# Kernel tuning notes

Hardware: AMD Instinct MI355X
Metric: run time of the kernel (lower is better)

The kernel has to match this reference:

```python
import jax, jax.numpy as jnp
import numpy as np

B, F_SIZE, DIM = 2048, 32, 64
LAYER_SIZES = (128, 128)


def setup_inputs() -> dict:
    key = jax.random.key(0)
    k1, k2, k3 = jax.random.split(key, 3)
    inputs = jax.random.normal(k1, (B, F_SIZE, DIM), dtype=jnp.float32)
    # Conv1d(kernel=1) weights: (out_channels, in_channels)
    W0 = jax.random.normal(k2, (128, F_SIZE * F_SIZE), dtype=jnp.float32) * 0.03
    b0 = jnp.zeros((128,), dtype=jnp.float32)
    # split_half -> field_nums[1] = 64 -> in_channels = 64 * 32 = 2048
    W1 = jax.random.normal(k3, (128, 64 * F_SIZE), dtype=jnp.float32) * 0.03
    b1 = jnp.zeros((128,), dtype=jnp.float32)
    return {"inputs": inputs, "W0": W0, "b0": b0, "W1": W1, "b1": b1}


def _cin_forward(inputs, Ws, bs):
    batch, _, dim = inputs.shape
    x0 = inputs
    h = inputs
    finals = []
    n_layers = len(Ws)
    for i in range(n_layers):
        H = h.shape[1]
        M = x0.shape[1]
        # outer-product interaction: (b, H, M, d) -> (b, H*M, d)
        z = jnp.einsum('bhd,bmd->bhmd', h, x0).reshape(batch, H * M, dim)
        # 1x1 conv == per-position channel matmul
        out = jnp.einsum('bcd,oc->bod', z, Ws[i]) + bs[i][None, :, None]
        out = jax.nn.relu(out)
        size = Ws[i].shape[0]
        if i != n_layers - 1:
            # split_half: first half feeds next layer, second half is output
            h = out[:, : size // 2, :]
            finals.append(out[:, size // 2 :, :])
        else:
            finals.append(out)
    result = jnp.concatenate(finals, axis=1)  # (b, 64 + 128, d)
    return jnp.sum(result, axis=-1)           # (b, 192)


def reference(inputs, W0, b0, W1, b1):
    return _cin_forward(inputs, (W0, W1), (b0, b1))
```

## Files before the change

kernel.cpp:

```cpp
#include <hip/hip_runtime.h>


#define BATCH 2048
#define FSZ   32
#define DIM   64
#define K0    1024
#define K1    2048
#define OUTC  192

#define W0_ELEMS (128 * K0)
#define W1_ELEMS (128 * K1)
#define TOT_ELEMS (W0_ELEMS + W1_ELEMS)
#define CVT_THREADS (TOT_ELEMS / 4)

typedef _Float16 v8h __attribute__((ext_vector_type(8)));
typedef _Float16 v4h __attribute__((ext_vector_type(4)));
typedef float    v4f __attribute__((ext_vector_type(4)));

#define XT_PITCH 40

__global__ void convert_w_kernel(const float* __restrict__ W0,
                                 const float* __restrict__ W1,
                                 _Float16* __restrict__ wsw) {
    int t = blockIdx.x * blockDim.x + threadIdx.x;
    if (t >= CVT_THREADS) return;
    int e = t * 4;
    const float* src;
    _Float16* dst;
    if (e < W0_ELEMS) {
        int j0 = e & 7, lane = (e >> 3) & 63, s = (e >> 9) & 7, ks = e >> 12;
        src = W0 + (size_t)(s * 16 + (lane & 15)) * K0
                 + ks * 32 + (lane >> 4) * 8 + j0;
        dst = wsw + e;
    } else {
        int u = e - W0_ELEMS;
        int j0 = u & 7, lane = (u >> 3) & 63, s = (u >> 9) & 7, ks = u >> 12;
        src = W1 + (size_t)(s * 16 + (lane & 15)) * K1
                 + ks * 32 + (lane >> 4) * 8 + j0;
        dst = wsw + W0_ELEMS + u;
    }
    float4 v = *(const float4*)src;
    dst[0] = (_Float16)v.x;
    dst[1] = (_Float16)v.y;
    dst[2] = (_Float16)v.z;
    dst[3] = (_Float16)v.w;
}

__global__ __launch_bounds__(256, 4) void cin_kernel(
    const float* __restrict__ X,
    const float* __restrict__ b0,
    const float* __restrict__ b1,
    const _Float16* __restrict__ Wsw,
    float* __restrict__ out)
{
    __shared__ _Float16 xT[2][DIM * XT_PITCH];
    __shared__ _Float16 xS[2][FSZ * 64];
    __shared__ _Float16 h1S[2][64 * 64];

    const int b0i  = blockIdx.x * 2;
    const int tid  = threadIdx.x;
    const int wave = tid >> 6;
    const int lane = tid & 63;
    const int p    = wave & 1;
    const int rh   = wave >> 1;
    const int quad = lane >> 4;
    const int col  = lane & 15;

    #pragma unroll
    for (int i = 0; i < 4; ++i) {
        int idx = tid + i * 256;
        int pp = idx >> 9, r4 = idx & 511;
        float4 v = *(const float4*)(X + (size_t)(b0i + pp) * (FSZ * DIM) + r4 * 4);
        int m = (r4 * 4) >> 6, d = (r4 * 4) & 63;
        int tq = d >> 4, cc = d & 15;
        _Float16 f0 = (_Float16)v.x, f1 = (_Float16)v.y,
                 f2 = (_Float16)v.z, f3 = (_Float16)v.w;
        xT[pp][(d + 0) * XT_PITCH + m] = f0;
        xT[pp][(d + 1) * XT_PITCH + m] = f1;
        xT[pp][(d + 2) * XT_PITCH + m] = f2;
        xT[pp][(d + 3) * XT_PITCH + m] = f3;
        xS[pp][m * 64 + (cc + 0) * 4 + tq] = f0;
        xS[pp][m * 64 + (cc + 1) * 4 + tq] = f1;
        xS[pp][m * 64 + (cc + 2) * 4 + tq] = f2;
        xS[pp][m * 64 + (cc + 3) * 4 + tq] = f3;
    }
    __syncthreads();

    v8h xv8[4];
    #pragma unroll
    for (int t = 0; t < 4; ++t)
        xv8[t] = *(const v8h*)(&xT[p][(16 * t + col) * XT_PITCH + quad * 8]);

    const _Float16* WbL0 = Wsw + (size_t)rh * 2048 + (size_t)lane * 8;
    const _Float16* Wb   = Wsw + (size_t)(rh * 4) * 512 + (size_t)lane * 8;
    const _Float16* xSp  = &xS[p][col * 4];
    const _Float16* h1Sp = &h1S[p][col * 4];
    (void)WbL0;

    v4f acc[4][4];
    #pragma unroll
    for (int f = 0; f < 4; ++f)
        #pragma unroll
        for (int t = 0; t < 4; ++t) acc[f][t] = (v4f)0.0f;

    {
        v8h aC[4], aN[4];
        v4h svC, svN;
        #pragma unroll
        for (int i = 0; i < 4; ++i) aC[i] = *(const v8h*)(Wb + i * 512);
        svC = *(const v4h*)(xSp);
        #pragma unroll 2
        for (int ks = 0; ks < 32; ++ks) {
            const int kn = (ks + 1) & 31;
            const _Float16* Wn = Wb + (size_t)kn * 4096;
            #pragma unroll
            for (int i = 0; i < 4; ++i) aN[i] = *(const v8h*)(Wn + i * 512);
            svN = *(const v4h*)(xSp + kn * 64);
            __builtin_amdgcn_s_setprio(1);
            #pragma unroll
            for (int t = 0; t < 4; ++t) {
                _Float16 s = svC[t];
                v8h s8 = {s, s, s, s, s, s, s, s};
                v8h bfr = s8 * xv8[t];
                acc[0][t] = __builtin_amdgcn_mfma_f32_16x16x32_f16(aC[0], bfr, acc[0][t], 0, 0, 0);
                acc[1][t] = __builtin_amdgcn_mfma_f32_16x16x32_f16(aC[1], bfr, acc[1][t], 0, 0, 0);
                acc[2][t] = __builtin_amdgcn_mfma_f32_16x16x32_f16(aC[2], bfr, acc[2][t], 0, 0, 0);
                acc[3][t] = __builtin_amdgcn_mfma_f32_16x16x32_f16(aC[3], bfr, acc[3][t], 0, 0, 0);
            }
            __builtin_amdgcn_s_setprio(0);
            #pragma unroll
            for (int i = 0; i < 4; ++i) aC[i] = aN[i];
            svC = svN;
        }
    }

    if (rh == 0) {
        #pragma unroll
        for (int f = 0; f < 4; ++f) {
            #pragma unroll
            for (int reg = 0; reg < 4; ++reg) {
                const int o = f * 16 + quad * 4 + reg;
                const float bias = b0[o];
                v4h pk;
                #pragma unroll
                for (int t = 0; t < 4; ++t) {
                    float v = acc[f][t][reg] + bias;
                    v = v > 0.0f ? v : 0.0f;
                    pk[t] = (_Float16)v;
                }
                *(v4h*)(&h1S[p][o * 64 + col * 4]) = pk;
            }
        }
    } else {
        #pragma unroll
        for (int f = 0; f < 4; ++f) {
            #pragma unroll
            for (int reg = 0; reg < 4; ++reg) {
                const int o = 64 + f * 16 + quad * 4 + reg;
                const float bias = b0[o];
                float s = 0.0f;
                #pragma unroll
                for (int t = 0; t < 4; ++t) {
                    float v = acc[f][t][reg] + bias;
                    s += (v > 0.0f ? v : 0.0f);
                }
                s += __shfl_xor(s, 1);
                s += __shfl_xor(s, 2);
                s += __shfl_xor(s, 4);
                s += __shfl_xor(s, 8);
                if (col == 0) out[(size_t)(b0i + p) * OUTC + (o - 64)] = s;
            }
        }
    }
    __syncthreads();

    #pragma unroll
    for (int f = 0; f < 4; ++f)
        #pragma unroll
        for (int t = 0; t < 4; ++t) acc[f][t] = (v4f)0.0f;

    {
        const _Float16* Wb1 = Wsw + W0_ELEMS + (size_t)(rh * 4) * 512 + (size_t)lane * 8;
        v8h aC[4], aN[4];
        v4h svC, svN;
        #pragma unroll
        for (int i = 0; i < 4; ++i) aC[i] = *(const v8h*)(Wb1 + i * 512);
        svC = *(const v4h*)(h1Sp);
        #pragma unroll 2
        for (int ks = 0; ks < 64; ++ks) {
            const int kn = (ks + 1) & 63;
            const _Float16* Wn = Wb1 + (size_t)kn * 4096;
            #pragma unroll
            for (int i = 0; i < 4; ++i) aN[i] = *(const v8h*)(Wn + i * 512);
            svN = *(const v4h*)(h1Sp + kn * 64);
            __builtin_amdgcn_s_setprio(1);
            #pragma unroll
            for (int t = 0; t < 4; ++t) {
                _Float16 s = svC[t];
                v8h s8 = {s, s, s, s, s, s, s, s};
                v8h bfr = s8 * xv8[t];
                acc[0][t] = __builtin_amdgcn_mfma_f32_16x16x32_f16(aC[0], bfr, acc[0][t], 0, 0, 0);
                acc[1][t] = __builtin_amdgcn_mfma_f32_16x16x32_f16(aC[1], bfr, acc[1][t], 0, 0, 0);
                acc[2][t] = __builtin_amdgcn_mfma_f32_16x16x32_f16(aC[2], bfr, acc[2][t], 0, 0, 0);
                acc[3][t] = __builtin_amdgcn_mfma_f32_16x16x32_f16(aC[3], bfr, acc[3][t], 0, 0, 0);
            }
            __builtin_amdgcn_s_setprio(0);
            #pragma unroll
            for (int i = 0; i < 4; ++i) aC[i] = aN[i];
            svC = svN;
        }
    }

    #pragma unroll
    for (int f = 0; f < 4; ++f) {
        #pragma unroll
        for (int reg = 0; reg < 4; ++reg) {
            const int o = rh * 64 + f * 16 + quad * 4 + reg;
            const float bias = b1[o];
            float s = 0.0f;
            #pragma unroll
            for (int t = 0; t < 4; ++t) {
                float v = acc[f][t][reg] + bias;
                s += (v > 0.0f ? v : 0.0f);
            }
            s += __shfl_xor(s, 1);
            s += __shfl_xor(s, 2);
            s += __shfl_xor(s, 4);
            s += __shfl_xor(s, 8);
            if (col == 0) out[(size_t)(b0i + p) * OUTC + 64 + o] = s;
        }
    }
}

extern "C" void kernel_launch(void* const* d_in, const int* in_sizes, int n_in,
                              void* d_out, int out_size, void* d_ws, size_t ws_size,
                              hipStream_t stream) {
    const float* X  = (const float*)d_in[0];
    const float* W0 = (const float*)d_in[1];
    const float* b0 = (const float*)d_in[2];
    const float* W1 = (const float*)d_in[3];
    const float* b1 = (const float*)d_in[4];
    float* out = (float*)d_out;
    _Float16* wsw = (_Float16*)d_ws;

    convert_w_kernel<<<(CVT_THREADS + 255) / 256, 256, 0, stream>>>(W0, W1, wsw);
    cin_kernel<<<BATCH / 2, 256, 0, stream>>>(X, b0, b1, wsw, out);
}
```

Before: 149.8 us.

## Split layer-1 GEMM across waves by d-tiles instead of output channels

```diff
diff --git a/kernel.cpp b/kernel.cpp
--- a/kernel.cpp
+++ b/kernel.cpp
@@ -15,6 +15,7 @@
 
 typedef _Float16 v8h __attribute__((ext_vector_type(8)));
 typedef _Float16 v4h __attribute__((ext_vector_type(4)));
+typedef _Float16 v2h __attribute__((ext_vector_type(2)));
 typedef float    v4f __attribute__((ext_vector_type(4)));
 
 #define XT_PITCH 40
@@ -46,6 +47,10 @@
     dst[3] = (_Float16)v.w;
 }
 
+__device__ __forceinline__ v4f mfma16(v8h a, v8h b, v4f c) {
+    return __builtin_amdgcn_mfma_f32_16x16x32_f16(a, b, c, 0, 0, 0);
+}
+
 __global__ __launch_bounds__(256, 4) void cin_kernel(
     const float* __restrict__ X,
     const float* __restrict__ b0,
@@ -56,6 +61,7 @@
     __shared__ _Float16 xT[2][DIM * XT_PITCH];
     __shared__ _Float16 xS[2][FSZ * 64];
     __shared__ _Float16 h1S[2][64 * 64];
+    __shared__ float    pbuf[2][2][128];
 
     const int b0i  = blockIdx.x * 2;
     const int tid  = threadIdx.x;
@@ -91,11 +97,8 @@
     for (int t = 0; t < 4; ++t)
         xv8[t] = *(const v8h*)(&xT[p][(16 * t + col) * XT_PITCH + quad * 8]);
 
-    const _Float16* WbL0 = Wsw + (size_t)rh * 2048 + (size_t)lane * 8;
     const _Float16* Wb   = Wsw + (size_t)(rh * 4) * 512 + (size_t)lane * 8;
     const _Float16* xSp  = &xS[p][col * 4];
-    const _Float16* h1Sp = &h1S[p][col * 4];
-    (void)WbL0;
 
     v4f acc[4][4];
     #pragma unroll
@@ -116,18 +119,16 @@
             #pragma unroll
             for (int i = 0; i < 4; ++i) aN[i] = *(const v8h*)(Wn + i * 512);
             svN = *(const v4h*)(xSp + kn * 64);
-            __builtin_amdgcn_s_setprio(1);
             #pragma unroll
             for (int t = 0; t < 4; ++t) {
                 _Float16 s = svC[t];
                 v8h s8 = {s, s, s, s, s, s, s, s};
                 v8h bfr = s8 * xv8[t];
-                acc[0][t] = __builtin_amdgcn_mfma_f32_16x16x32_f16(aC[0], bfr, acc[0][t], 0, 0, 0);
-                acc[1][t] = __builtin_amdgcn_mfma_f32_16x16x32_f16(aC[1], bfr, acc[1][t], 0, 0, 0);
-                acc[2][t] = __builtin_amdgcn_mfma_f32_16x16x32_f16(aC[2], bfr, acc[2][t], 0, 0, 0);
-                acc[3][t] = __builtin_amdgcn_mfma_f32_16x16x32_f16(aC[3], bfr, acc[3][t], 0, 0, 0);
+                acc[0][t] = mfma16(aC[0], bfr, acc[0][t]);
+                acc[1][t] = mfma16(aC[1], bfr, acc[1][t]);
+                acc[2][t] = mfma16(aC[2], bfr, acc[2][t]);
+                acc[3][t] = mfma16(aC[3], bfr, acc[3][t]);
             }
-            __builtin_amdgcn_s_setprio(0);
             #pragma unroll
             for (int i = 0; i < 4; ++i) aC[i] = aN[i];
             svC = svN;
@@ -174,61 +175,86 @@
     }
     __syncthreads();
 
-    #pragma unroll
-    for (int f = 0; f < 4; ++f)
-        #pragma unroll
-        for (int t = 0; t < 4; ++t) acc[f][t] = (v4f)0.0f;
+    v8h xw0 = (rh == 0) ? xv8[0] : xv8[2];
+    v8h xw1 = (rh == 0) ? xv8[1] : xv8[3];
+
+    v4f a1[8][2];
+    #pragma unroll
+    for (int f = 0; f < 8; ++f) {
+        a1[f][0] = (v4f)0.0f;
+        a1[f][1] = (v4f)0.0f;
+    }
 
     {
-        const _Float16* Wb1 = Wsw + W0_ELEMS + (size_t)(rh * 4) * 512 + (size_t)lane * 8;
-        v8h aC[4], aN[4];
-        v4h svC, svN;
-        #pragma unroll
-        for (int i = 0; i < 4; ++i) aC[i] = *(const v8h*)(Wb1 + i * 512);
-        svC = *(const v4h*)(h1Sp);
-        #pragma unroll 2
+        const _Float16* Wb1 = Wsw + W0_ELEMS + (size_t)lane * 8;
+        const _Float16* hSp = &h1S[p][col * 4 + rh * 2];
+        v8h G0, G1, G2, G3, H0, H1, H2, H3;
+        v2h svC, svN;
+        G0 = *(const v8h*)(Wb1);
+        G1 = *(const v8h*)(Wb1 + 512);
+        G2 = *(const v8h*)(Wb1 + 1024);
+        G3 = *(const v8h*)(Wb1 + 1536);
+        svC = *(const v2h*)(hSp);
+        #pragma unroll 1
         for (int ks = 0; ks < 64; ++ks) {
             const int kn = (ks + 1) & 63;
+            const _Float16* Wc = Wb1 + (size_t)ks * 4096;
             const _Float16* Wn = Wb1 + (size_t)kn * 4096;
-            #pragma unroll
-            for (int i = 0; i < 4; ++i) aN[i] = *(const v8h*)(Wn + i * 512);
-            svN = *(const v4h*)(h1Sp + kn * 64);
-            __builtin_amdgcn_s_setprio(1);
-            #pragma unroll
-            for (int t = 0; t < 4; ++t) {
-                _Float16 s = svC[t];
-                v8h s8 = {s, s, s, s, s, s, s, s};
-                v8h bfr = s8 * xv8[t];
-                acc[0][t] = __builtin_amdgcn_mfma_f32_16x16x32_f16(aC[0], bfr, acc[0][t], 0, 0, 0);
-                acc[1][t] = __builtin_amdgcn_mfma_f32_16x16x32_f16(aC[1], bfr, acc[1][t], 0, 0, 0);
-                acc[2][t] = __builtin_amdgcn_mfma_f32_16x16x32_f16(aC[2], bfr, acc[2][t], 0, 0, 0);
-                acc[3][t] = __builtin_amdgcn_mfma_f32_16x16x32_f16(aC[3], bfr, acc[3][t], 0, 0, 0);
-            }
-            __builtin_amdgcn_s_setprio(0);
-            #pragma unroll
-            for (int i = 0; i < 4; ++i) aC[i] = aN[i];
+            H0 = *(const v8h*)(Wc + 2048);
+            H1 = *(const v8h*)(Wc + 2560);
+            H2 = *(const v8h*)(Wc + 3072);
+            H3 = *(const v8h*)(Wc + 3584);
+            svN = *(const v2h*)(hSp + kn * 64);
+            _Float16 s0 = svC[0], s1 = svC[1];
+            v8h s08 = {s0, s0, s0, s0, s0, s0, s0, s0};
+            v8h s18 = {s1, s1, s1, s1, s1, s1, s1, s1};
+            v8h bf0 = s08 * xw0;
+            v8h bf1 = s18 * xw1;
+            a1[0][0] = mfma16(G0, bf0, a1[0][0]);
+            a1[0][1] = mfma16(G0, bf1, a1[0][1]);
+            a1[1][0] = mfma16(G1, bf0, a1[1][0]);
+            a1[1][1] = mfma16(G1, bf1, a1[1][1]);
+            a1[2][0] = mfma16(G2, bf0, a1[2][0]);
+            a1[2][1] = mfma16(G2, bf1, a1[2][1]);
+            a1[3][0] = mfma16(G3, bf0, a1[3][0]);
+            a1[3][1] = mfma16(G3, bf1, a1[3][1]);
+            G0 = *(const v8h*)(Wn);
+            G1 = *(const v8h*)(Wn + 512);
+            G2 = *(const v8h*)(Wn + 1024);
+            G3 = *(const v8h*)(Wn + 1536);
+            a1[4][0] = mfma16(H0, bf0, a1[4][0]);
+            a1[4][1] = mfma16(H0, bf1, a1[4][1]);
+            a1[5][0] = mfma16(H1, bf0, a1[5][0]);
+            a1[5][1] = mfma16(H1, bf1, a1[5][1]);
+            a1[6][0] = mfma16(H2, bf0, a1[6][0]);
+            a1[6][1] = mfma16(H2, bf1, a1[6][1]);
+            a1[7][0] = mfma16(H3, bf0, a1[7][0]);
+            a1[7][1] = mfma16(H3, bf1, a1[7][1]);
             svC = svN;
         }
     }
 
     #pragma unroll
-    for (int f = 0; f < 4; ++f) {
+    for (int f = 0; f < 8; ++f) {
         #pragma unroll
         for (int reg = 0; reg < 4; ++reg) {
-            const int o = rh * 64 + f * 16 + quad * 4 + reg;
+            const int o = f * 16 + quad * 4 + reg;
             const float bias = b1[o];
-            float s = 0.0f;
-            #pragma unroll
-            for (int t = 0; t < 4; ++t) {
-                float v = acc[f][t][reg] + bias;
-                s += (v > 0.0f ? v : 0.0f);
-            }
+            float v0 = a1[f][0][reg] + bias; v0 = v0 > 0.0f ? v0 : 0.0f;
+            float v1 = a1[f][1][reg] + bias; v1 = v1 > 0.0f ? v1 : 0.0f;
+            float s = v0 + v1;
             s += __shfl_xor(s, 1);
             s += __shfl_xor(s, 2);
             s += __shfl_xor(s, 4);
             s += __shfl_xor(s, 8);
-            if (col == 0) out[(size_t)(b0i + p) * OUTC + 64 + o] = s;
-        }
+            if (col == 0) pbuf[p][rh][o] = s;
+        }
+    }
+    __syncthreads();
+    if (rh == 0) {
+        float* op = out + (size_t)(b0i + p) * OUTC + 64;
+        op[lane]      = pbuf[p][0][lane]      + pbuf[p][1][lane];
+        op[64 + lane] = pbuf[p][0][64 + lane] + pbuf[p][1][64 + lane];
     }
 }
 
```

Result: slower. 172.0 us (+14.8%).
